# Optimization experiments

Hardware: AMD Instinct MI355X
Metric: run time of the kernel (lower is better)

The kernel has to match this reference:

```python
import jax, jax.numpy as jnp
import numpy as np
import math

B, S, E = 4, 2048, 1024

def setup_inputs() -> dict:
    key = jax.random.key(0)
    ks = jax.random.split(key, 12)
    scale = 1.0 / math.sqrt(E)
    inp = {
        "query": jax.random.normal(ks[0], (B, S, E), jnp.float32),
        "key_": jax.random.normal(ks[1], (B, S, E), jnp.float32),
        "value": jax.random.normal(ks[2], (B, S, E), jnp.float32),
        # causal mask, broadcast over batch: 1 = keep, 0 = mask
        "mask": jnp.broadcast_to(jnp.tril(jnp.ones((S, S), jnp.int32)), (B, S, S)),
        "Wq": jax.random.uniform(ks[3], (E, E), jnp.float32, -scale, scale),
        "bq": jax.random.uniform(ks[4], (E,), jnp.float32, -scale, scale),
        "Wk": jax.random.uniform(ks[5], (E, E), jnp.float32, -scale, scale),
        "bk": jax.random.uniform(ks[6], (E,), jnp.float32, -scale, scale),
        "Wv": jax.random.uniform(ks[7], (E, E), jnp.float32, -scale, scale),
        "bv": jax.random.uniform(ks[8], (E,), jnp.float32, -scale, scale),
        "Wo": jax.random.uniform(ks[9], (E, E), jnp.float32, -scale, scale),
        "bo": jax.random.uniform(ks[10], (E,), jnp.float32, -scale, scale),
    }
    return inp

def reference(query, key_, value, mask, Wq, bq, Wk, bk, Wv, bv, Wo, bo):
    # Linear projections (torch Linear: x @ W.T + b)
    Q = jnp.einsum('bse,fe->bsf', query, Wq) + bq
    K = jnp.einsum('bse,fe->bsf', key_, Wk) + bk
    V = jnp.einsum('bse,fe->bsf', value, Wv) + bv
    # NOTE: module never splits heads; scores over full embed_dim, scaled by sqrt(embed_dim)
    scores = jnp.einsum('bqe,bke->bqk', Q, K) / jnp.sqrt(jnp.asarray(E, Q.dtype))
    scores = jnp.where(mask == 0, -jnp.inf, scores)
    attn = jax.nn.softmax(scores, axis=-1)
    attn_out = jnp.einsum('bqk,bke->bqe', attn, V)
    return jnp.einsum('bse,fe->bsf', attn_out, Wo) + bo
```

## Files before the change

kernel.cpp:

```cpp
#include <hip/hip_runtime.h>

typedef __bf16 bf16;
typedef __attribute__((ext_vector_type(8))) __bf16 bf16x8;
typedef __attribute__((ext_vector_type(4))) __bf16 bf16x4;
typedef __attribute__((ext_vector_type(4))) float f32x4;

#define DEVINL __device__ __forceinline__

DEVINL void gload_lds16(const bf16* g, bf16* l) {
    __builtin_amdgcn_global_load_lds(
        (__attribute__((address_space(1))) unsigned int*)(unsigned long long)g,
        (__attribute__((address_space(3))) unsigned int*)l,
        16, 0, 0);
}

__global__ __launch_bounds__(256) void cvt3_f32_to_bf16(
    const float* __restrict__ a, const float* __restrict__ b,
    const float* __restrict__ c, bf16* __restrict__ out, int n4) {
    int i = blockIdx.x * blockDim.x + threadIdx.x;
    if (i >= n4) return;
    const float* src = (blockIdx.z == 0) ? a : (blockIdx.z == 1) ? b : c;
    bf16* dst = out + (size_t)blockIdx.z * (size_t)n4 * 4;
    float4 f = ((const float4*)src)[i];
    bf16x4 o;
    o.x = (bf16)f.x; o.y = (bf16)f.y; o.z = (bf16)f.z; o.w = (bf16)f.w;
    ((bf16x4*)dst)[i] = o;
}

__global__ __launch_bounds__(256) void cvt4_f32_to_bf16(
    const float* __restrict__ a, const float* __restrict__ b,
    const float* __restrict__ c, const float* __restrict__ d,
    bf16* __restrict__ out, int n4) {
    int i = blockIdx.x * blockDim.x + threadIdx.x;
    if (i >= n4) return;
    const float* src = (blockIdx.z == 0) ? a : (blockIdx.z == 1) ? b
                     : (blockIdx.z == 2) ? c : d;
    bf16* dst = out + (size_t)blockIdx.z * (size_t)n4 * 4;
    float4 f = ((const float4*)src)[i];
    bf16x4 o;
    o.x = (bf16)f.x; o.y = (bf16)f.y; o.z = (bf16)f.z; o.w = (bf16)f.w;
    ((bf16x4*)dst)[i] = o;
}

__global__ __launch_bounds__(256) void transpose_bf16(
    const unsigned short* __restrict__ in, unsigned short* __restrict__ out,
    int R, int C) {
    __shared__ unsigned short t[64][65];
    const size_t bo = (size_t)blockIdx.z * R * C;
    const int r0 = blockIdx.y * 64, c0 = blockIdx.x * 64;
#pragma unroll
    for (int i = 0; i < 16; i++) {
        int lin = threadIdx.x + i * 256;
        int r = lin >> 6, c = lin & 63;
        t[r][c] = in[bo + (size_t)(r0 + r) * C + (c0 + c)];
    }
    __syncthreads();
#pragma unroll
    for (int i = 0; i < 16; i++) {
        int lin = threadIdx.x + i * 256;
        int r = lin >> 6, c = lin & 63;
        out[bo + (size_t)(c0 + r) * R + (r0 + c)] = t[c][r];
    }
}

template <int EPI>
__global__ __launch_bounds__(256) void gemm_bt128(
    const bf16* __restrict__ A, const bf16* __restrict__ B,
    const float* __restrict__ bias, void* __restrict__ Cv,
    int M, int N, int K,
    long long sA, long long sB, long long sC, long long sBias,
    float scale) {
    const int bx = blockIdx.x, by = blockIdx.y, bz = blockIdx.z;
    const int m0 = by * 128, n0 = bx * 128;

    A += (size_t)bz * sA;
    B += (size_t)bz * sB;
    if (bias) bias += (size_t)bz * sBias;

    __shared__ __align__(16) bf16 As[128 * 32];
    __shared__ __align__(16) bf16 Bs[128 * 32];

    const int tid = threadIdx.x;
    const int wave = tid >> 6;
    const int lane = tid & 63;
    const int lr = lane & 15;
    const int lq = lane >> 4;
    const int wm = (wave >> 1) * 64;
    const int wn = (wave & 1) * 64;
    const int srow = lane >> 2;
    const int scol = (lane & 3) * 8;

    f32x4 acc[4][4];
    const f32x4 fzero = {0.f, 0.f, 0.f, 0.f};
#pragma unroll
    for (int i = 0; i < 4; i++)
#pragma unroll
        for (int j = 0; j < 4; j++) acc[i][j] = fzero;

    for (int k0 = 0; k0 < K; k0 += 32) {
        const bf16* ga0 = A + (size_t)(m0 + wave * 16 + srow) * K + (k0 + scol);
        const bf16* gb0 = B + (size_t)(n0 + wave * 16 + srow) * K + (k0 + scol);
        gload_lds16(ga0,                  As + wave * 512);
        gload_lds16(ga0 + (size_t)64 * K, As + (wave + 4) * 512);
        gload_lds16(gb0,                  Bs + wave * 512);
        gload_lds16(gb0 + (size_t)64 * K, Bs + (wave + 4) * 512);
        __syncthreads();

        bf16x8 af[4], bfr[4];
#pragma unroll
        for (int i = 0; i < 4; i++)
            af[i] = *(const bf16x8*)(As + (wm + i * 16 + lr) * 32 + lq * 8);
#pragma unroll
        for (int j = 0; j < 4; j++)
            bfr[j] = *(const bf16x8*)(Bs + (wn + j * 16 + lr) * 32 + lq * 8);
#pragma unroll
        for (int i = 0; i < 4; i++)
#pragma unroll
            for (int j = 0; j < 4; j++)
                acc[i][j] = __builtin_amdgcn_mfma_f32_16x16x32_bf16(
                    af[i], bfr[j], acc[i][j], 0, 0, 0);
        __syncthreads();
    }

#pragma unroll
    for (int j = 0; j < 4; j++) {
        const int col = n0 + wn + j * 16 + lr;
        const float bb = bias ? bias[col] : 0.0f;
#pragma unroll
        for (int i = 0; i < 4; i++) {
            const int rowb = m0 + wm + i * 16 + lq * 4;
#pragma unroll
            for (int r = 0; r < 4; r++) {
                if (EPI == 0)
                    ((bf16*)Cv)[(size_t)bz * sC + (size_t)(rowb + r) * N + col] =
                        (bf16)(acc[i][j][r] * scale + bb);
                else
                    ((float*)Cv)[(size_t)bz * sC + (size_t)(rowb + r) * N + col] =
                        acc[i][j][r] * scale + bb;
            }
        }
    }
}

template <int EPI>
__global__ __launch_bounds__(256) void gemm_bt64(
    const bf16* __restrict__ A, const bf16* __restrict__ B,
    const float* __restrict__ bias, void* __restrict__ Cv,
    int M, int N, int K,
    long long sA, long long sB, long long sC, long long sBias,
    float scale, int causal) {
    const int bx = blockIdx.x, by = blockIdx.y, bz = blockIdx.z;
    const int m0 = by * 128, n0 = bx * 64;
    if (causal == 1 && n0 > m0 + 127) return;
    int Keff = K;
    if (causal == 2) { Keff = m0 + 128; if (Keff > K) Keff = K; }

    A += (size_t)bz * sA;
    B += (size_t)bz * sB;
    if (bias) bias += (size_t)bz * sBias;

    __shared__ __align__(16) bf16 As[2][128 * 32];
    __shared__ __align__(16) bf16 Bs[2][64 * 32];

    const int tid = threadIdx.x;
    const int wave = tid >> 6;
    const int lane = tid & 63;
    const int lr = lane & 15;
    const int lq = lane >> 4;
    const int wm = wave * 32;
    const int srow = lane >> 2;
    const int scol = (lane & 3) * 8;

    f32x4 acc[2][4];
    const f32x4 fzero = {0.f, 0.f, 0.f, 0.f};
#pragma unroll
    for (int i = 0; i < 2; i++)
#pragma unroll
        for (int j = 0; j < 4; j++) acc[i][j] = fzero;

    for (int k0 = 0; k0 < Keff; k0 += 64) {
#pragma unroll
        for (int kc = 0; kc < 2; kc++) {
            const bf16* ga0 =
                A + (size_t)(m0 + wave * 16 + srow) * K + (k0 + kc * 32 + scol);
            const bf16* gb0 =
                B + (size_t)(n0 + wave * 16 + srow) * K + (k0 + kc * 32 + scol);
            gload_lds16(ga0,                  As[kc] + wave * 512);
            gload_lds16(ga0 + (size_t)64 * K, As[kc] + (wave + 4) * 512);
            gload_lds16(gb0,                  Bs[kc] + wave * 512);
        }
        __syncthreads();

        bf16x8 af[2][2], bfr[2][4];
#pragma unroll
        for (int kc = 0; kc < 2; kc++) {
#pragma unroll
            for (int i = 0; i < 2; i++)
                af[kc][i] = *(const bf16x8*)(As[kc] + (wm + i * 16 + lr) * 32 + lq * 8);
#pragma unroll
            for (int j = 0; j < 4; j++)
                bfr[kc][j] = *(const bf16x8*)(Bs[kc] + (j * 16 + lr) * 32 + lq * 8);
        }
#pragma unroll
        for (int kc = 0; kc < 2; kc++)
#pragma unroll
            for (int i = 0; i < 2; i++)
#pragma unroll
                for (int j = 0; j < 4; j++)
                    acc[i][j] = __builtin_amdgcn_mfma_f32_16x16x32_bf16(
                        af[kc][i], bfr[kc][j], acc[i][j], 0, 0, 0);
        __syncthreads();
    }

#pragma unroll
    for (int j = 0; j < 4; j++) {
        const int col = n0 + j * 16 + lr;
        const float bb = bias ? bias[col] : 0.0f;
#pragma unroll
        for (int i = 0; i < 2; i++) {
            const int rowb = m0 + wm + i * 16 + lq * 4;
#pragma unroll
            for (int r = 0; r < 4; r++) {
                if (EPI == 0)
                    ((bf16*)Cv)[(size_t)bz * sC + (size_t)(rowb + r) * N + col] =
                        (bf16)(acc[i][j][r] * scale + bb);
                else
                    ((float*)Cv)[(size_t)bz * sC + (size_t)(rowb + r) * N + col] =
                        acc[i][j][r] * scale + bb;
            }
        }
    }
}

__global__ __launch_bounds__(256) void softmax_causal(
    const float* __restrict__ Sc, bf16* __restrict__ P, int S) {
    const int row = blockIdx.x;
    const int q = row & (S - 1);
    const float* src = Sc + (size_t)row * S;
    bf16* dst = P + (size_t)row * S;
    const int L = q + 1;
    const int tid = threadIdx.x;

    float v[8];
    float mx = -3.0e38f;
#pragma unroll
    for (int i = 0; i < 8; i++) {
        int k = tid + i * 256;
        v[i] = (k < L) ? src[k] : -3.0e38f;
        mx = fmaxf(mx, v[i]);
    }
#pragma unroll
    for (int off = 32; off > 0; off >>= 1) mx = fmaxf(mx, __shfl_xor(mx, off, 64));
    __shared__ float redm[4], reds[4];
    if ((tid & 63) == 0) redm[tid >> 6] = mx;
    __syncthreads();
    mx = fmaxf(fmaxf(redm[0], redm[1]), fmaxf(redm[2], redm[3]));

    float sum = 0.f;
#pragma unroll
    for (int i = 0; i < 8; i++) {
        int k = tid + i * 256;
        float e = (k < L) ? __expf(v[i] - mx) : 0.f;
        v[i] = e;
        sum += e;
    }
#pragma unroll
    for (int off = 32; off > 0; off >>= 1) sum += __shfl_xor(sum, off, 64);
    if ((tid & 63) == 0) reds[tid >> 6] = sum;
    __syncthreads();
    sum = reds[0] + reds[1] + reds[2] + reds[3];
    const float inv = 1.0f / sum;
#pragma unroll
    for (int i = 0; i < 8; i++) {
        int k = tid + i * 256;
        dst[k] = (bf16)(v[i] * inv);
    }
}

extern "C" void kernel_launch(void* const* d_in, const int* in_sizes, int n_in,
                              void* d_out, int out_size, void* d_ws, size_t ws_size,
                              hipStream_t stream) {
    const int B = 4, S = 2048, E = 1024;
    const size_t SBE = (size_t)B * S * E;
    const size_t EE = (size_t)E * E;

    const float* q_in = (const float*)d_in[0];
    const float* k_in = (const float*)d_in[1];
    const float* v_in = (const float*)d_in[2];
    const float* Wq = (const float*)d_in[4];
    const float* bq = (const float*)d_in[5];
    const float* Wk = (const float*)d_in[6];
    const float* bk = (const float*)d_in[7];
    const float* Wv = (const float*)d_in[8];
    const float* bv = (const float*)d_in[9];
    const float* Wo = (const float*)d_in[10];
    const float* bo = (const float*)d_in[11];

    char* ws = (char*)d_ws;
    bf16* qkvb = (bf16*)ws;
    float* Sc = (float*)ws;
    bf16* AO = (bf16*)ws;
    char* p = ws + (size_t)B * S * S * 4;
    bf16* QKVb = (bf16*)p; p += 3 * SBE * 2;
    bf16* Vt = (bf16*)p; p += SBE * 2;
    bf16* Pb = (bf16*)p; p += (size_t)B * S * S * 2;
    bf16* Wb = (bf16*)p; p += 4 * EE * 2;
    float* biasWS = (float*)p; p += 3 * E * 4;

    bf16* Qb = QKVb;
    bf16* Vb = QKVb + 2 * SBE;
    bf16* Wob = Wb + 3 * EE;

    dim3 gcvt3((int)(SBE / 4 / 256), 1, 3);
    cvt3_f32_to_bf16<<<gcvt3, 256, 0, stream>>>(q_in, k_in, v_in, qkvb, (int)(SBE / 4));
    dim3 gcvt4((int)(EE / 4 / 256), 1, 4);
    cvt4_f32_to_bf16<<<gcvt4, 256, 0, stream>>>(Wq, Wk, Wv, Wo, Wb, (int)(EE / 4));
    hipMemcpyAsync(biasWS,         bq, E * 4, hipMemcpyDeviceToDevice, stream);
    hipMemcpyAsync(biasWS + E,     bk, E * 4, hipMemcpyDeviceToDevice, stream);
    hipMemcpyAsync(biasWS + 2 * E, bv, E * 4, hipMemcpyDeviceToDevice, stream);

    dim3 blk(256);
    dim3 gproj(E / 128, (B * S) / 128, 3);
    gemm_bt128<0><<<gproj, blk, 0, stream>>>(qkvb, Wb, biasWS, QKVb,
                                             B * S, E, E,
                                             (long long)SBE, (long long)EE,
                                             (long long)SBE, (long long)E, 1.f);

    dim3 gt(E / 64, S / 64, B);
    transpose_bf16<<<gt, blk, 0, stream>>>((const unsigned short*)Vb,
                                           (unsigned short*)Vt, S, E);

    dim3 gsc(S / 64, S / 128, B);
    gemm_bt64<1><<<gsc, blk, 0, stream>>>(Qb, QKVb + SBE, nullptr, Sc, S, S, E,
                                          (long long)S * E, (long long)S * E,
                                          (long long)S * S, 0, 0.03125f, 1);

    softmax_causal<<<B * S, 256, 0, stream>>>(Sc, Pb, S);

    dim3 gpv(E / 64, S / 128, B);
    gemm_bt64<0><<<gpv, blk, 0, stream>>>(Pb, Vt, nullptr, AO, S, E, S,
                                          (long long)S * S, (long long)E * S,
                                          (long long)S * E, 0, 1.f, 2);

    dim3 gout(E / 64, (B * S) / 128, 1);
    gemm_bt64<1><<<gout, blk, 0, stream>>>(AO, Wob, bo, (float*)d_out,
                                           B * S, E, E, 0, 0, 0, 0, 1.f, 0);
}
```

Baseline: 431.7 us.

## Store attention scores in bf16 and add XCD-aware block swizzle to GEMMs

The QK^T score matrix is now written as bf16 instead of fp32, and softmax reads and writes it with bf16x2 vector accesses. This halves the traffic of the largest intermediate. Separately, all GEMM kernels remap block indices so consecutive row tiles land on the same XCD, which should improve L2 reuse. Rounding scores to bf16 before softmax costs some accuracy.

Result: faster. 421.7 us (-2.3%).

```diff
diff --git a/kernel.cpp b/kernel.cpp
--- a/kernel.cpp
+++ b/kernel.cpp
@@ -3,6 +3,7 @@
 typedef __bf16 bf16;
 typedef __attribute__((ext_vector_type(8))) __bf16 bf16x8;
 typedef __attribute__((ext_vector_type(4))) __bf16 bf16x4;
+typedef __attribute__((ext_vector_type(2))) __bf16 bf16x2;
 typedef __attribute__((ext_vector_type(4))) float f32x4;
 
 #define DEVINL __device__ __forceinline__
@@ -12,6 +13,15 @@
         (__attribute__((address_space(1))) unsigned int*)(unsigned long long)g,
         (__attribute__((address_space(3))) unsigned int*)l,
         16, 0, 0);
+}
+
+DEVINL void xcd_swizzle(int& bx, int& by) {
+    const int gx = gridDim.x, gy = gridDim.y;
+    const int l = blockIdx.y * gx + blockIdx.x;
+    const int xcd = l & 7;
+    const int li = l >> 3;
+    by = xcd * (gy >> 3) + li / gx;
+    bx = li - (li / gx) * gx;
 }
 
 __global__ __launch_bounds__(256) void cvt3_f32_to_bf16(
@@ -70,7 +80,9 @@
     int M, int N, int K,
     long long sA, long long sB, long long sC, long long sBias,
     float scale) {
-    const int bx = blockIdx.x, by = blockIdx.y, bz = blockIdx.z;
+    int bx, by;
+    xcd_swizzle(bx, by);
+    const int bz = blockIdx.z;
     const int m0 = by * 128, n0 = bx * 128;
 
     A += (size_t)bz * sA;
@@ -149,7 +161,9 @@
     int M, int N, int K,
     long long sA, long long sB, long long sC, long long sBias,
     float scale, int causal) {
-    const int bx = blockIdx.x, by = blockIdx.y, bz = blockIdx.z;
+    int bx, by;
+    xcd_swizzle(bx, by);
+    const int bz = blockIdx.z;
     const int m0 = by * 128, n0 = bx * 64;
     if (causal == 1 && n0 > m0 + 127) return;
     int Keff = K;
@@ -233,10 +247,10 @@
 }
 
 __global__ __launch_bounds__(256) void softmax_causal(
-    const float* __restrict__ Sc, bf16* __restrict__ P, int S) {
+    const bf16* __restrict__ Sc, bf16* __restrict__ P, int S) {
     const int row = blockIdx.x;
     const int q = row & (S - 1);
-    const float* src = Sc + (size_t)row * S;
+    const bf16* src = Sc + (size_t)row * S;
     bf16* dst = P + (size_t)row * S;
     const int L = q + 1;
     const int tid = threadIdx.x;
@@ -244,10 +258,12 @@
     float v[8];
     float mx = -3.0e38f;
 #pragma unroll
-    for (int i = 0; i < 8; i++) {
-        int k = tid + i * 256;
-        v[i] = (k < L) ? src[k] : -3.0e38f;
-        mx = fmaxf(mx, v[i]);
+    for (int i = 0; i < 4; i++) {
+        int k = (i * 256 + tid) * 2;
+        bf16x2 u = ((const bf16x2*)src)[i * 256 + tid];
+        v[2 * i]     = (k < L)     ? (float)u.x : -3.0e38f;
+        v[2 * i + 1] = (k + 1 < L) ? (float)u.y : -3.0e38f;
+        mx = fmaxf(mx, fmaxf(v[2 * i], v[2 * i + 1]));
     }
 #pragma unroll
     for (int off = 32; off > 0; off >>= 1) mx = fmaxf(mx, __shfl_xor(mx, off, 64));
@@ -259,8 +275,7 @@
     float sum = 0.f;
 #pragma unroll
     for (int i = 0; i < 8; i++) {
-        int k = tid + i * 256;
-        float e = (k < L) ? __expf(v[i] - mx) : 0.f;
+        float e = (v[i] > -1.0e38f) ? __expf(v[i] - mx) : 0.f;
         v[i] = e;
         sum += e;
     }
@@ -271,9 +286,11 @@
     sum = reds[0] + reds[1] + reds[2] + reds[3];
     const float inv = 1.0f / sum;
 #pragma unroll
-    for (int i = 0; i < 8; i++) {
-        int k = tid + i * 256;
-        dst[k] = (bf16)(v[i] * inv);
+    for (int i = 0; i < 4; i++) {
+        bf16x2 o;
+        o.x = (bf16)(v[2 * i] * inv);
+        o.y = (bf16)(v[2 * i + 1] * inv);
+        ((bf16x2*)dst)[i * 256 + tid] = o;
     }
 }
 
@@ -298,7 +315,7 @@
 
     char* ws = (char*)d_ws;
     bf16* qkvb = (bf16*)ws;
-    float* Sc = (float*)ws;
+    bf16* Sc = (bf16*)ws;
     bf16* AO = (bf16*)ws;
     char* p = ws + (size_t)B * S * S * 4;
     bf16* QKVb = (bf16*)p; p += 3 * SBE * 2;
@@ -331,7 +348,7 @@
                                            (unsigned short*)Vt, S, E);
 
     dim3 gsc(S / 64, S / 128, B);
-    gemm_bt64<1><<<gsc, blk, 0, stream>>>(Qb, QKVb + SBE, nullptr, Sc, S, S, E,
+    gemm_bt64<0><<<gsc, blk, 0, stream>>>(Qb, QKVb + SBE, nullptr, Sc, S, S, E,
                                           (long long)S * E, (long long)S * E,
                                           (long long)S * S, 0, 0.03125f, 1);
 
```
